# Kernel optimization log

Measured on AMD Instinct MI355X. Metric: run time of the kernel, lower is better.

## Reference

```python
import jax, jax.numpy as jnp
import numpy as np

SPARSITY = 0.1
B, N, K = 256, 65536, 64

def setup_inputs() -> dict:
    key = jax.random.key(0)
    kx, kc = jax.random.split(key)
    x = jax.random.normal(kx, (B, N), dtype=jnp.float32)
    cluster_assignments = jax.random.randint(kc, (N,), 0, K, dtype=jnp.int32)
    cluster_weights = jnp.ones((K,), dtype=jnp.float32)
    return {"x": x, "cluster_weights": cluster_weights, "cluster_assignments": cluster_assignments}

def reference(x, cluster_weights, cluster_assignments):
    b, n = x.shape
    k = cluster_weights.shape[0]
    # cluster activation prob (context=None path): softmax(weights), same for all batch rows
    p = jax.nn.softmax(cluster_weights) * SPARSITY                      # [K]
    ku, kv = jax.random.split(jax.random.key(42))
    u = jax.random.uniform(ku, (b, n))   # drives the random permutation per (batch, cluster)
    v = jax.random.uniform(kv, (b, n))   # drives the binomial count (sum of Bernoullis)
    # Binomial(len(cluster_i), p_i) == sum of per-neuron Bernoulli(p_i) over the cluster
    bern = (v < p[cluster_assignments][None, :]).astype(jnp.int32)      # [B, N]
    counts = jax.vmap(lambda row: jax.ops.segment_sum(row, cluster_assignments, num_segments=k))(bern)  # [B, K]
    counts = jnp.maximum(counts, 1)                                     # max(1, binomial sample)
    # within-cluster uniform-random ranking: sort by (cluster, u); rank = pos - cluster_start
    sizes = jnp.bincount(cluster_assignments, length=k)                 # [K]
    starts = jnp.cumsum(sizes) - sizes                                  # exclusive cumsum [K]
    cluster_sorted = jnp.sort(cluster_assignments)                      # [N], batch-independent
    pos_in_cluster = jnp.arange(n) - starts[cluster_sorted]             # [N]
    keys = cluster_assignments.astype(jnp.float32)[None, :] + u * 0.999  # cluster-major composite key
    order = jnp.argsort(keys, axis=1)                                   # [B, N]
    mask_sorted = (pos_in_cluster[None, :] < counts[:, cluster_sorted]).astype(x.dtype)  # [B, N]
    mask = jnp.zeros_like(x).at[jnp.arange(b)[:, None], order].set(mask_sorted)
    return x * mask
```

## Files before the change

### kernel.cpp

```cpp
#include <hip/hip_runtime.h>
#include <stdint.h>

#define NROWS 256
#define NCOLS 65536
#define KCL   64
#define TMAX  20
#define NBLK  128
#define CHUNK (NCOLS / NBLK)
#define ZBLK  2048

__device__ __forceinline__ void tf2x32(uint32_t k0, uint32_t k1,
                                       uint32_t x0, uint32_t x1,
                                       uint32_t& o0, uint32_t& o1) {
  const uint32_t ks2 = k0 ^ k1 ^ 0x1BD11BDAu;
  x0 += k0; x1 += k1;
#define TFR(r) { x0 += x1; x1 = (x1 << (r)) | (x1 >> (32 - (r))); x1 ^= x0; }
  TFR(13) TFR(15) TFR(26) TFR(6)
  x0 += k1; x1 += ks2 + 1u;
  TFR(17) TFR(29) TFR(16) TFR(24)
  x0 += ks2; x1 += k0 + 2u;
  TFR(13) TFR(15) TFR(26) TFR(6)
  x0 += k0; x1 += k1 + 3u;
  TFR(17) TFR(29) TFR(16) TFR(24)
  x0 += k1; x1 += ks2 + 4u;
  TFR(13) TFR(15) TFR(26) TFR(6)
  x0 += ks2; x1 += k0 + 5u;
#undef TFR
  o0 = x0; o1 = x1;
}

__device__ __forceinline__ uint32_t jax_bits(uint32_t k0, uint32_t k1, uint32_t f) {
  uint32_t o0, o1;
  tf2x32(k0, k1, 0u, f, o0, o1);
  return o0 ^ o1;
}

__device__ __forceinline__ float bits_to_u01(uint32_t bits) {
  return __uint_as_float((bits >> 9) | 0x3f800000u) - 1.0f;
}

__device__ __forceinline__ float key_from_ubits(uint32_t ubits, float kf) {
  return __fadd_rn(kf, __fmul_rn(bits_to_u01(ubits), 0.999f));
}

__device__ __forceinline__ int wave_sum_i(int v) {
#pragma unroll
  for (int m = 1; m < 64; m <<= 1) v += __shfl_xor(v, m, 64);
  return v;
}
__device__ __forceinline__ uint32_t wave_min_u(uint32_t v) {
#pragma unroll
  for (int m = 1; m < 64; m <<= 1) {
    const uint32_t o = (uint32_t)__shfl_xor((int)v, m, 64);
    v = (o < v) ? o : v;
  }
  return v;
}
__device__ __forceinline__ int wave_min_i(int v) {
#pragma unroll
  for (int m = 1; m < 64; m <<= 1) {
    const int o = __shfl_xor(v, m, 64);
    v = (o < v) ? o : v;
  }
  return v;
}

__global__ __launch_bounds__(256)
void k_zerohist(float4* __restrict__ outv, const int* __restrict__ a,
                int* __restrict__ blockhist) {
  const int gtid = blockIdx.x * 256 + threadIdx.x;
  const float4 z = make_float4(0.f, 0.f, 0.f, 0.f);
#pragma unroll
  for (int i = 0; i < 8; ++i)
    outv[gtid + i * (ZBLK * 256)] = z;
  if (blockIdx.x < NBLK) {
    __shared__ int h[KCL];
    if (threadIdx.x < KCL) h[threadIdx.x] = 0;
    __syncthreads();
    const int base = blockIdx.x * CHUNK;
#pragma unroll
    for (int i = base + threadIdx.x; i < base + CHUNK; i += 256)
      atomicAdd(&h[a[i]], 1);
    __syncthreads();
    if (threadIdx.x < KCL) blockhist[blockIdx.x * KCL + threadIdx.x] = h[threadIdx.x];
  }
}

__global__ void k_prefix_setup(int* __restrict__ blockhist, int* __restrict__ sizes,
                               int* __restrict__ starts,
                               const float* __restrict__ w, uint32_t* __restrict__ hdr,
                               uint32_t* __restrict__ vthresh) {
  const int k = threadIdx.x;
  int acc = 0;
#pragma unroll 8
  for (int blk = 0; blk < NBLK; ++blk) {
    const int t = blockhist[blk * KCL + k];
    blockhist[blk * KCL + k] = acc;
    acc += t;
  }
  sizes[k] = acc;
  int scan = acc;
#pragma unroll
  for (int d = 1; d < 64; d <<= 1) {
    const int o = __shfl_up(scan, d, 64);
    if (k >= d) scan += o;
  }
  starts[k] = scan - acc;
  const float wk = w[k];
  float m = wk;
#pragma unroll
  for (int d = 1; d < 64; d <<= 1) m = fmaxf(m, __shfl_xor(m, d, 64));
  const float e = expf(wk - m);
  float s = e;
#pragma unroll
  for (int d = 1; d < 64; d <<= 1) s += __shfl_xor(s, d, 64);
  const float pk = (e / s) * 0.1f;
  vthresh[k] = (uint32_t)ceilf(pk * 8388608.0f);
  if (k == 0) {
    uint32_t o0, o1;
    tf2x32(0u, 42u, 0u, 0u, o0, o1); hdr[0] = o0; hdr[1] = o1;
    tf2x32(0u, 42u, 0u, 1u, o0, o1); hdr[2] = o0; hdr[3] = o1;
  }
}

__global__ __launch_bounds__(256)
void k_scatter(const int* __restrict__ a, const int* __restrict__ blockhist,
               const int* __restrict__ starts, int* __restrict__ idx_sorted) {
  __shared__ int cur[KCL];
  const int tid = threadIdx.x;
  if (tid < KCL) cur[tid] = starts[tid] + blockhist[blockIdx.x * KCL + tid];
  __syncthreads();
  const int base = blockIdx.x * CHUNK;
#pragma unroll
  for (int i = base + tid; i < base + CHUNK; i += 256) {
    const int k = a[i];
    const int slot = atomicAdd(&cur[k], 1);
    idx_sorted[slot] = i;
  }
}

__global__ __launch_bounds__(256)
void k_select(const float* __restrict__ x,
              const int* __restrict__ idx_sorted,
              const int* __restrict__ sizes,
              const int* __restrict__ starts,
              const uint32_t* __restrict__ hdr,
              const uint32_t* __restrict__ vthresh,
              float* __restrict__ out) {
  const int lane = threadIdx.x & 63;
  const int pair = (blockIdx.x << 2) + (threadIdx.x >> 6);
  const int b = pair & (NROWS - 1);
  const int k = pair >> 8;

  int sz = sizes[k];
  const int st = starts[k];
  if (sz <= 0) return;
  if (sz > TMAX * 64) sz = TMAX * 64;

  const uint32_t ku0 = hdr[0], ku1 = hdr[1], kv0 = hdr[2], kv1 = hdr[3];
  const uint32_t vt = vthresh[k];
  const float kf = (float)k;
  const uint32_t bbase = (uint32_t)(b << 16);

  int nv[TMAX];
#pragma unroll
  for (int t = 0; t < TMAX; ++t) {
    const int j = lane + (t << 6);
    nv[t] = (j < sz) ? idx_sorted[st + j] : 0;
  }

  uint32_t kb[TMAX];
  uint32_t curmin = 0xFFFFFFFFu;
  int cnt = 0;
#pragma unroll
  for (int t = 0; t < TMAX; ++t) {
    const int j = lane + (t << 6);
    uint32_t kbv = 0xFFFFFFFFu;
    if (j < sz) {
      const uint32_t f = bbase + (uint32_t)nv[t];
      const uint32_t ubv = jax_bits(ku0, ku1, f);
      const uint32_t vbv = jax_bits(kv0, kv1, f);
      cnt += ((vbv >> 9) < vt) ? 1 : 0;
      kbv = __float_as_uint(key_from_ubits(ubv, kf));
    }
    kb[t] = kbv;
    curmin = (kbv < curmin) ? kbv : curmin;
  }
  int C = wave_sum_i(cnt);
  if (C < 1) C = 1;

  uint32_t consumed = 0;
  uint32_t Tkey;
  for (int e = 0;; ++e) {
    const uint32_t wmn = wave_min_u(curmin);
    if (e == C - 1) { Tkey = wmn; break; }
    const unsigned long long bal = __ballot(curmin == wmn);
    const int src = (int)__ffsll((long long)bal) - 1;
    if (lane == src) {
      int ct = -1;
#pragma unroll
      for (int t = 0; t < TMAX; ++t)
        if (ct < 0 && !((consumed >> t) & 1u) && kb[t] == wmn) ct = t;
      consumed |= (1u << ct);
      uint32_t nm = 0xFFFFFFFFu;
#pragma unroll
      for (int t = 0; t < TMAX; ++t) {
        const uint32_t v = ((consumed >> t) & 1u) ? 0xFFFFFFFFu : kb[t];
        nm = (v < nm) ? v : nm;
      }
      curmin = nm;
    }
  }

  int packed = 0;
#pragma unroll
  for (int t = 0; t < TMAX; ++t) {
    packed += (kb[t] < Tkey) ? (1 << 16) : 0;
    packed += (kb[t] == Tkey) ? 1 : 0;
  }
  const int sred = wave_sum_i(packed);
  const int nbelow = sred >> 16;
  const int tieCnt = sred & 0xFFFF;
  const int r = C - nbelow;

  int cutN = 0x7FFFFFFF;
  if (r < tieCnt) {
    uint32_t cons2 = 0;
    for (int e = 0; e < r; ++e) {
      int mnN = 0x7FFFFFFF, mnT = 0;
#pragma unroll
      for (int t = 0; t < TMAX; ++t) {
        if (kb[t] == Tkey && !(cons2 & (1u << t))) {
          const int n = idx_sorted[st + lane + (t << 6)];
          if (n < mnN) { mnN = n; mnT = t; }
        }
      }
      const int w = wave_min_i(mnN);
      cutN = w;
      const unsigned long long bal = __ballot(mnN == w);
      const int src = (int)__ffsll((long long)bal) - 1;
      if (lane == src) cons2 |= (1u << mnT);
    }
  }

  const size_t rowoff = (size_t)b * NCOLS;
#pragma unroll
  for (int t = 0; t < TMAX; ++t) {
    const uint32_t v = kb[t];
    bool sel = (v < Tkey);
    if (!sel && v == Tkey) {
      if (r >= tieCnt) {
        sel = true;
      } else {
        const int n = idx_sorted[st + lane + (t << 6)];
        sel = (n <= cutN);
      }
    }
    if (sel) {
      const int n = idx_sorted[st + lane + (t << 6)];
      const size_t off = rowoff + (uint32_t)n;
      out[off] = x[off];
    }
  }
}

extern "C" void kernel_launch(void* const* d_in, const int* in_sizes, int n_in,
                              void* d_out, int out_size, void* d_ws, size_t ws_size,
                              hipStream_t stream) {
  const float* x = (const float*)d_in[0];
  const float* w = (const float*)d_in[1];
  const int* assign = (const int*)d_in[2];
  float* out = (float*)d_out;
  uint32_t* ws = (uint32_t*)d_ws;

  uint32_t* hdr       = ws;
  uint32_t* vthresh   = ws + 4;
  int*      sizes     = (int*)(ws + 68);
  int*      starts    = (int*)(ws + 132);
  int*      blockhist = (int*)(ws + 196);
  int*      idxs      = (int*)(ws + 196 + NBLK * KCL);

  k_zerohist<<<ZBLK, 256, 0, stream>>>((float4*)out, assign, blockhist);
  k_prefix_setup<<<1, 64, 0, stream>>>(blockhist, sizes, starts, w, hdr, vthresh);
  k_scatter<<<NBLK, 256, 0, stream>>>(assign, blockhist, starts, idxs);
  k_select<<<(NROWS * KCL) / 4, 256, 0, stream>>>(x, idxs, sizes, starts, hdr, vthresh, out);
  (void)n_in; (void)in_sizes; (void)ws_size;
}
```

Measured before the change: 105.3 us.

## Drop separate output zero-fill; write zeros for unselected elements in select kernel

Removes the full-output zeroing pass, so the first kernel only builds the histogram. The select kernel now writes every element of its cluster: `x` for selected positions and zero for the rest. The tie-break and final pass use the cluster indices already held in registers instead of reloading them from `idx_sorted`. This avoids one dense write of the output, but replaces it with about 16M scattered 4-byte stores whose columns are interleaved across clusters. It also depends on every cluster fitting within the TMAX*64 cap, since any element beyond the cap is never written.

Measured after the change: 193.9 us. +84.2%, slower.

```diff
diff --git a/kernel.cpp b/kernel.cpp
--- a/kernel.cpp
+++ b/kernel.cpp
@@ -7,7 +7,6 @@
 #define TMAX  20
 #define NBLK  128
 #define CHUNK (NCOLS / NBLK)
-#define ZBLK  2048
 
 __device__ __forceinline__ void tf2x32(uint32_t k0, uint32_t k1,
                                        uint32_t x0, uint32_t x1,
@@ -66,24 +65,17 @@
 }
 
 __global__ __launch_bounds__(256)
-void k_zerohist(float4* __restrict__ outv, const int* __restrict__ a,
-                int* __restrict__ blockhist) {
-  const int gtid = blockIdx.x * 256 + threadIdx.x;
-  const float4 z = make_float4(0.f, 0.f, 0.f, 0.f);
-#pragma unroll
-  for (int i = 0; i < 8; ++i)
-    outv[gtid + i * (ZBLK * 256)] = z;
-  if (blockIdx.x < NBLK) {
-    __shared__ int h[KCL];
-    if (threadIdx.x < KCL) h[threadIdx.x] = 0;
-    __syncthreads();
-    const int base = blockIdx.x * CHUNK;
-#pragma unroll
-    for (int i = base + threadIdx.x; i < base + CHUNK; i += 256)
-      atomicAdd(&h[a[i]], 1);
-    __syncthreads();
-    if (threadIdx.x < KCL) blockhist[blockIdx.x * KCL + threadIdx.x] = h[threadIdx.x];
-  }
+void k_hist(const int* __restrict__ a, int* __restrict__ blockhist) {
+  __shared__ int h[KCL];
+  const int tid = threadIdx.x;
+  if (tid < KCL) h[tid] = 0;
+  __syncthreads();
+  const int base = blockIdx.x * CHUNK;
+#pragma unroll
+  for (int i = base + tid; i < base + CHUNK; i += 256)
+    atomicAdd(&h[a[i]], 1);
+  __syncthreads();
+  if (tid < KCL) blockhist[blockIdx.x * KCL + tid] = h[tid];
 }
 
 __global__ void k_prefix_setup(int* __restrict__ blockhist, int* __restrict__ sizes,
@@ -230,9 +222,8 @@
       int mnN = 0x7FFFFFFF, mnT = 0;
 #pragma unroll
       for (int t = 0; t < TMAX; ++t) {
-        if (kb[t] == Tkey && !(cons2 & (1u << t))) {
-          const int n = idx_sorted[st + lane + (t << 6)];
-          if (n < mnN) { mnN = n; mnT = t; }
+        if (kb[t] == Tkey && !((cons2 >> t) & 1u)) {
+          if (nv[t] < mnN) { mnN = nv[t]; mnT = t; }
         }
       }
       const int w = wave_min_i(mnN);
@@ -244,22 +235,18 @@
   }
 
   const size_t rowoff = (size_t)b * NCOLS;
-#pragma unroll
-  for (int t = 0; t < TMAX; ++t) {
-    const uint32_t v = kb[t];
-    bool sel = (v < Tkey);
-    if (!sel && v == Tkey) {
-      if (r >= tieCnt) {
-        sel = true;
-      } else {
-        const int n = idx_sorted[st + lane + (t << 6)];
-        sel = (n <= cutN);
-      }
-    }
-    if (sel) {
-      const int n = idx_sorted[st + lane + (t << 6)];
-      const size_t off = rowoff + (uint32_t)n;
-      out[off] = x[off];
+  const bool allTies = (r >= tieCnt);
+#pragma unroll
+  for (int t = 0; t < TMAX; ++t) {
+    const int j = lane + (t << 6);
+    if (j < sz) {
+      const uint32_t v = kb[t];
+      bool sel = (v < Tkey);
+      if (!sel && v == Tkey) sel = allTies ? true : (nv[t] <= cutN);
+      const size_t off = rowoff + (uint32_t)nv[t];
+      float val = 0.0f;
+      if (sel) val = x[off];
+      out[off] = val;
     }
   }
 }
@@ -280,7 +267,7 @@
   int*      blockhist = (int*)(ws + 196);
   int*      idxs      = (int*)(ws + 196 + NBLK * KCL);
 
-  k_zerohist<<<ZBLK, 256, 0, stream>>>((float4*)out, assign, blockhist);
+  k_hist<<<NBLK, 256, 0, stream>>>(assign, blockhist);
   k_prefix_setup<<<1, 64, 0, stream>>>(blockhist, sizes, starts, w, hdr, vthresh);
   k_scatter<<<NBLK, 256, 0, stream>>>(assign, blockhist, starts, idxs);
   k_select<<<(NROWS * KCL) / 4, 256, 0, stream>>>(x, idxs, sizes, starts, hdr, vthresh, out);
```

## Fuse prefix setup into scatter kernel and fold RNG keys to compile-time constants

Applied to the files above, without the earlier changes.

The single-block prefix/softmax kernel is removed. Each scatter block now redundantly computes its own per-cluster offsets from the block histograms, and block 0 writes sizes, starts and the Bernoulli thresholds. The threefry key derivation for the fixed seed is computed at compile time, and the select kernel reuses register-held indices instead of reloading idx_sorted. This removes one launch and some global reloads, in exchange for every scatter block reading the full histogram array.

Measured after the change: 98.80 us, median of 2. 1.07x faster.

```diff
diff --git a/kernel.cpp b/kernel.cpp
--- a/kernel.cpp
+++ b/kernel.cpp
@@ -29,6 +29,27 @@
   o0 = x0; o1 = x1;
 }
 
+struct TFO { uint32_t a, b; };
+constexpr TFO tf_const(uint32_t k0, uint32_t k1, uint32_t x0, uint32_t x1) {
+  const uint32_t ks2 = k0 ^ k1 ^ 0x1BD11BDAu;
+  x0 += k0; x1 += k1;
+#define TFC(r) { x0 += x1; x1 = (x1 << (r)) | (x1 >> (32 - (r))); x1 ^= x0; }
+  TFC(13) TFC(15) TFC(26) TFC(6)
+  x0 += k1; x1 += ks2 + 1u;
+  TFC(17) TFC(29) TFC(16) TFC(24)
+  x0 += ks2; x1 += k0 + 2u;
+  TFC(13) TFC(15) TFC(26) TFC(6)
+  x0 += k0; x1 += k1 + 3u;
+  TFC(17) TFC(29) TFC(16) TFC(24)
+  x0 += k1; x1 += ks2 + 4u;
+  TFC(13) TFC(15) TFC(26) TFC(6)
+  x0 += ks2; x1 += k0 + 5u;
+#undef TFC
+  return {x0, x1};
+}
+constexpr TFO KU = tf_const(0u, 42u, 0u, 0u);
+constexpr TFO KV = tf_const(0u, 42u, 0u, 1u);
+
 __device__ __forceinline__ uint32_t jax_bits(uint32_t k0, uint32_t k1, uint32_t f) {
   uint32_t o0, o1;
   tf2x32(k0, k1, 0u, f, o0, o1);
@@ -86,51 +107,49 @@
   }
 }
 
-__global__ void k_prefix_setup(int* __restrict__ blockhist, int* __restrict__ sizes,
-                               int* __restrict__ starts,
-                               const float* __restrict__ w, uint32_t* __restrict__ hdr,
-                               uint32_t* __restrict__ vthresh) {
-  const int k = threadIdx.x;
-  int acc = 0;
-#pragma unroll 8
-  for (int blk = 0; blk < NBLK; ++blk) {
-    const int t = blockhist[blk * KCL + k];
-    blockhist[blk * KCL + k] = acc;
-    acc += t;
-  }
-  sizes[k] = acc;
-  int scan = acc;
-#pragma unroll
-  for (int d = 1; d < 64; d <<= 1) {
-    const int o = __shfl_up(scan, d, 64);
-    if (k >= d) scan += o;
-  }
-  starts[k] = scan - acc;
-  const float wk = w[k];
-  float m = wk;
-#pragma unroll
-  for (int d = 1; d < 64; d <<= 1) m = fmaxf(m, __shfl_xor(m, d, 64));
-  const float e = expf(wk - m);
-  float s = e;
-#pragma unroll
-  for (int d = 1; d < 64; d <<= 1) s += __shfl_xor(s, d, 64);
-  const float pk = (e / s) * 0.1f;
-  vthresh[k] = (uint32_t)ceilf(pk * 8388608.0f);
-  if (k == 0) {
-    uint32_t o0, o1;
-    tf2x32(0u, 42u, 0u, 0u, o0, o1); hdr[0] = o0; hdr[1] = o1;
-    tf2x32(0u, 42u, 0u, 1u, o0, o1); hdr[2] = o0; hdr[3] = o1;
-  }
-}
-
 __global__ __launch_bounds__(256)
-void k_scatter(const int* __restrict__ a, const int* __restrict__ blockhist,
-               const int* __restrict__ starts, int* __restrict__ idx_sorted) {
+void k_prescatter(const int* __restrict__ a, const int* __restrict__ blockhist,
+                  int* __restrict__ sizes_g, int* __restrict__ starts_g,
+                  const float* __restrict__ w, uint32_t* __restrict__ vthresh,
+                  int* __restrict__ idx_sorted) {
   __shared__ int cur[KCL];
   const int tid = threadIdx.x;
-  if (tid < KCL) cur[tid] = starts[tid] + blockhist[blockIdx.x * KCL + tid];
+  const int lane = tid & 63;
+  const int wid = tid >> 6;
+  const int blk = blockIdx.x;
+
+  if (wid == 0) {
+    int own = 0, tot = 0;
+#pragma unroll 8
+    for (int b2 = 0; b2 < NBLK; ++b2) {
+      const int h = blockhist[b2 * KCL + lane];
+      own += (b2 < blk) ? h : 0;
+      tot += h;
+    }
+    int scan = tot;
+#pragma unroll
+    for (int d = 1; d < 64; d <<= 1) {
+      const int o = __shfl_up(scan, d, 64);
+      if (lane >= d) scan += o;
+    }
+    const int start = scan - tot;
+    cur[lane] = start + own;
+    if (blk == 0) {
+      sizes_g[lane] = tot;
+      starts_g[lane] = start;
+      const float wk = w[lane];
+      float m = wk;
+#pragma unroll
+      for (int d = 1; d < 64; d <<= 1) m = fmaxf(m, __shfl_xor(m, d, 64));
+      const float e = expf(wk - m);
+      float s = e;
+#pragma unroll
+      for (int d = 1; d < 64; d <<= 1) s += __shfl_xor(s, d, 64);
+      vthresh[lane] = (uint32_t)ceilf((e / s) * 0.1f * 8388608.0f);
+    }
+  }
   __syncthreads();
-  const int base = blockIdx.x * CHUNK;
+  const int base = blk * CHUNK;
 #pragma unroll
   for (int i = base + tid; i < base + CHUNK; i += 256) {
     const int k = a[i];
@@ -144,7 +163,6 @@
               const int* __restrict__ idx_sorted,
               const int* __restrict__ sizes,
               const int* __restrict__ starts,
-              const uint32_t* __restrict__ hdr,
               const uint32_t* __restrict__ vthresh,
               float* __restrict__ out) {
   const int lane = threadIdx.x & 63;
@@ -157,7 +175,7 @@
   if (sz <= 0) return;
   if (sz > TMAX * 64) sz = TMAX * 64;
 
-  const uint32_t ku0 = hdr[0], ku1 = hdr[1], kv0 = hdr[2], kv1 = hdr[3];
+  const uint32_t ku0 = KU.a, ku1 = KU.b, kv0 = KV.a, kv1 = KV.b;
   const uint32_t vt = vthresh[k];
   const float kf = (float)k;
   const uint32_t bbase = (uint32_t)(b << 16);
@@ -230,9 +248,8 @@
       int mnN = 0x7FFFFFFF, mnT = 0;
 #pragma unroll
       for (int t = 0; t < TMAX; ++t) {
-        if (kb[t] == Tkey && !(cons2 & (1u << t))) {
-          const int n = idx_sorted[st + lane + (t << 6)];
-          if (n < mnN) { mnN = n; mnT = t; }
+        if (kb[t] == Tkey && !((cons2 >> t) & 1u)) {
+          if (nv[t] < mnN) { mnN = nv[t]; mnT = t; }
         }
       }
       const int w = wave_min_i(mnN);
@@ -244,21 +261,14 @@
   }
 
   const size_t rowoff = (size_t)b * NCOLS;
+  const bool allTies = (r >= tieCnt);
 #pragma unroll
   for (int t = 0; t < TMAX; ++t) {
     const uint32_t v = kb[t];
     bool sel = (v < Tkey);
-    if (!sel && v == Tkey) {
-      if (r >= tieCnt) {
-        sel = true;
-      } else {
-        const int n = idx_sorted[st + lane + (t << 6)];
-        sel = (n <= cutN);
-      }
-    }
+    if (!sel && v == Tkey) sel = allTies ? true : (nv[t] <= cutN);
     if (sel) {
-      const int n = idx_sorted[st + lane + (t << 6)];
-      const size_t off = rowoff + (uint32_t)n;
+      const size_t off = rowoff + (uint32_t)nv[t];
       out[off] = x[off];
     }
   }
@@ -273,16 +283,16 @@
   float* out = (float*)d_out;
   uint32_t* ws = (uint32_t*)d_ws;
 
-  uint32_t* hdr       = ws;
-  uint32_t* vthresh   = ws + 4;
-  int*      sizes     = (int*)(ws + 68);
-  int*      starts    = (int*)(ws + 132);
-  int*      blockhist = (int*)(ws + 196);
-  int*      idxs      = (int*)(ws + 196 + NBLK * KCL);
+  uint32_t* vthresh   = ws;
+  int*      sizes     = (int*)(ws + 64);
+  int*      starts    = (int*)(ws + 128);
+  int*      blockhist = (int*)(ws + 192);
+  int*      idxs      = (int*)(ws + 192 + NBLK * KCL);
 
   k_zerohist<<<ZBLK, 256, 0, stream>>>((float4*)out, assign, blockhist);
-  k_prefix_setup<<<1, 64, 0, stream>>>(blockhist, sizes, starts, w, hdr, vthresh);
-  k_scatter<<<NBLK, 256, 0, stream>>>(assign, blockhist, starts, idxs);
-  k_select<<<(NROWS * KCL) / 4, 256, 0, stream>>>(x, idxs, sizes, starts, hdr, vthresh, out);
+  k_prescatter<<<NBLK, 256, 0, stream>>>(assign, blockhist, sizes, starts, w,
+                                         vthresh, idxs);
+  k_select<<<(NROWS * KCL) / 4, 256, 0, stream>>>(x, idxs, sizes, starts,
+                                                  vthresh, out);
   (void)n_in; (void)in_sizes; (void)ws_size;
 }
```
